# Kernel tuning notes

Measured on AMD Instinct MI355X. Metric: run time of the kernel, lower is better.

Reference implementation:

```python
import jax, jax.numpy as jnp
import numpy as np

B, N, C = 4, 2048, 512
H, D, L = 8, 64, 64  # num_heads, per-head dim, lunchbox_dim
SCALE = max(D, L) ** (-0.5)

def setup_inputs() -> dict:
    key = jax.random.key(0)
    k1, k2, k3, k4 = jax.random.split(key, 4)
    x = jax.random.normal(k1, (B, N, C), dtype=jnp.float32)
    v = jax.random.normal(k2, (N, H, L), dtype=jnp.float32) * (1.0 / np.sqrt(N))
    qkv = jax.random.normal(k3, (C, D * 2 * H), dtype=jnp.float32) * (1.0 / np.sqrt(C))
    proj = jax.random.normal(k4, (H * L, D), dtype=jnp.float32) * (1.0 / np.sqrt(H * L))
    return {"x": x, "v": v, "qkv": qkv, "proj": proj}

def reference(x, v, qkv, proj):
    # x: [B,N,C] -> [B,N,H,2,D]
    h = jnp.einsum('bnc,cd->bnd', x, qkv).reshape(B, N, H, 2, D)
    q = h[:, :, :, 0, :]  # [B,N,H,D]
    k = h[:, :, :, 1, :]  # [B,N,H,D]
    # attention scores [B,H,N,N]; NOTE: original code calls tf.nn.softmax but
    # discards the result, so no softmax is applied (faithful reproduction).
    attn = jnp.einsum('bnhd,bmhd->bhnm', q, k) * SCALE
    # contract with batch-independent lunchbox V: [B,H,N,N] x [N,H,L] -> [B,N,H,L]
    res = jnp.einsum('bhnm,mhl->bnhl', attn, v).reshape(B, N, H * L)
    out = jnp.einsum('bnc,cd->bnd', res, proj)  # [B,N,D]
    return out
```

## Files before the change

### kernel.cpp

```cpp
#include <hip/hip_runtime.h>
#include <hip/hip_bf16.h>


using f32x4 = __attribute__((ext_vector_type(4))) float;
using s16x8 = __attribute__((ext_vector_type(8))) short;

__device__ __forceinline__ unsigned short f2bf(float f) {
  unsigned int i;
  __builtin_memcpy(&i, &f, 4);
  unsigned int lsb = (i >> 16) & 1u;
  i += 0x7fffu + lsb;
  return (unsigned short)(i >> 16);
}
__device__ __forceinline__ float bf2f(unsigned short u) {
  unsigned int i = ((unsigned int)u) << 16;
  float f;
  __builtin_memcpy(&f, &i, 4);
  return f;
}
__device__ __forceinline__ void async_cp16(const void* g, void* l) {
  __builtin_amdgcn_global_load_lds((const __attribute__((address_space(1))) void*)g,
                                   (__attribute__((address_space(3))) void*)l, 16, 0, 0);
}

__global__ void k_convert_x(const float* __restrict__ x, unsigned short* __restrict__ xb) {
  size_t i = ((size_t)blockIdx.x * 256 + threadIdx.x) * 8;
  f32x4 a = *(const f32x4*)(x + i);
  f32x4 b = *(const f32x4*)(x + i + 4);
  ushort4 lo, hi;
  lo.x = f2bf(a[0]); lo.y = f2bf(a[1]); lo.z = f2bf(a[2]); lo.w = f2bf(a[3]);
  hi.x = f2bf(b[0]); hi.y = f2bf(b[1]); hi.z = f2bf(b[2]); hi.w = f2bf(b[3]);
  *(ushort4*)(xb + i) = lo;
  *(ushort4*)(xb + i + 4) = hi;
}

__global__ void k_transpose_qkv(const float* __restrict__ qkv,
                                unsigned short* __restrict__ qkvT) {
  __shared__ float tile[32][33];
  int j0 = blockIdx.x * 32;
  int c0 = blockIdx.y * 32;
  int tx = threadIdx.x, ty = threadIdx.y;
#pragma unroll
  for (int i = 0; i < 32; i += 8)
    tile[ty + i][tx] = qkv[(size_t)(c0 + ty + i) * 1024 + j0 + tx];
  __syncthreads();
  int h = j0 >> 7, s = (j0 >> 6) & 1, d0 = j0 & 63;
  int jp0 = s * 512 + h * 64 + d0;
#pragma unroll
  for (int i = 0; i < 32; i += 8)
    qkvT[(size_t)(jp0 + ty + i) * 512 + c0 + tx] = f2bf(tile[tx][ty + i]);
}

__global__ void k_gemm1(const unsigned short* __restrict__ A,
                        const unsigned short* __restrict__ Bt,
                        unsigned short* __restrict__ Qws,
                        unsigned short* __restrict__ Kws) {
  __shared__ unsigned short As[128 * 64];
  __shared__ unsigned short Bs[128 * 64];
  const int m0 = blockIdx.x * 128;
  const int n0 = blockIdx.y * 128;
  const int tid = threadIdx.x;
  const int lane = tid & 63;
  const int wave = tid >> 6;
  const int wm = wave >> 1, wn = wave & 1;

  f32x4 acc[4][4] = {};

  const int rstage = wave * 32 + (lane >> 3);
  const int cstage = (lane & 7) * 8;

  for (int kt = 0; kt < 512; kt += 64) {
    __syncthreads();
#pragma unroll
    for (int i = 0; i < 4; ++i) {
      async_cp16(A + (size_t)(m0 + rstage + i * 8) * 512 + kt + cstage,
                 As + (wave * 32 + i * 8) * 64);
      async_cp16(Bt + (size_t)(n0 + rstage + i * 8) * 512 + kt + cstage,
                 Bs + (wave * 32 + i * 8) * 64);
    }
    __syncthreads();
#pragma unroll
    for (int kk = 0; kk < 64; kk += 32) {
      s16x8 af[4], bfr[4];
#pragma unroll
      for (int i = 0; i < 4; ++i)
        af[i] = *(const s16x8*)(As + (wm * 64 + i * 16 + (lane & 15)) * 64 + kk + (lane >> 4) * 8);
#pragma unroll
      for (int j = 0; j < 4; ++j)
        bfr[j] = *(const s16x8*)(Bs + (wn * 64 + j * 16 + (lane & 15)) * 64 + kk + (lane >> 4) * 8);
#pragma unroll
      for (int i = 0; i < 4; ++i)
#pragma unroll
        for (int j = 0; j < 4; ++j)
          acc[i][j] = __builtin_amdgcn_mfma_f32_16x16x32_bf16(af[i], bfr[j], acc[i][j], 0, 0, 0);
    }
  }
  const int n_base = n0 + wn * 64;
#pragma unroll
  for (int i = 0; i < 4; ++i) {
    int grow = m0 + wm * 64 + i * 16 + (lane >> 4) * 4;
#pragma unroll
    for (int j = 0; j < 4; ++j) {
      int gcol = n_base + j * 16 + (lane & 15);
      unsigned short* dst;
      float scale;
      if (gcol < 512) { dst = Qws; scale = 0.125f; }
      else            { dst = Kws; gcol -= 512; scale = 1.0f; }
#pragma unroll
      for (int r = 0; r < 4; ++r)
        dst[(size_t)(grow + r) * 512 + gcol] = f2bf(acc[i][j][r] * scale);
    }
  }
}

__global__ void k_kv_partial(const unsigned short* __restrict__ Kws,
                             const float* __restrict__ v,
                             float* __restrict__ KVp) {
  const int wg = blockIdx.x;
  const int chunk = wg & 15;
  const int h = (wg >> 4) & 7;
  const int b = wg >> 7;
  __shared__ unsigned short Ks[128 * 64];
  __shared__ float Vs[128 * 64];
  const int tid = threadIdx.x;
  const int lane = tid & 63;
  const int wave = tid >> 6;
  const int n0 = chunk * 128;
  {
    const int r = wave * 32 + (lane >> 3);
    const int c = (lane & 7) * 8;
#pragma unroll
    for (int i = 0; i < 4; ++i)
      async_cp16(Kws + (size_t)(b * 2048 + n0 + r + i * 8) * 512 + h * 64 + c,
                 Ks + (wave * 32 + i * 8) * 64);
  }
  {
    const int r = wave * 32 + (lane >> 4);
    const int c = (lane & 15) * 4;
#pragma unroll
    for (int i = 0; i < 8; ++i)
      async_cp16(v + (size_t)(n0 + r + i * 4) * 512 + h * 64 + c,
                 Vs + (wave * 32 + i * 4) * 64);
  }
  __syncthreads();
  const int dq0 = (tid & 15) * 4;
  const int l0 = (tid >> 4) * 4;
  float acc[4][4] = {};
#pragma unroll 4
  for (int n = 0; n < 128; ++n) {
    ushort4 ku = *(const ushort4*)(Ks + n * 64 + dq0);
    f32x4 va = *(const f32x4*)(Vs + n * 64 + l0);
    float ka[4] = {bf2f(ku.x), bf2f(ku.y), bf2f(ku.z), bf2f(ku.w)};
#pragma unroll
    for (int a = 0; a < 4; ++a)
#pragma unroll
      for (int c = 0; c < 4; ++c)
        acc[a][c] += ka[a] * va[c];
  }
  float* dst = KVp + (size_t)wg * 4096;
#pragma unroll
  for (int a = 0; a < 4; ++a) {
    f32x4 o;
    o[0] = acc[a][0]; o[1] = acc[a][1]; o[2] = acc[a][2]; o[3] = acc[a][3];
    *(f32x4*)(dst + (dq0 + a) * 64 + l0) = o;
  }
}

__global__ void k_kv_reduce_w(const float* __restrict__ KVp,
                              const float* __restrict__ proj,
                              unsigned short* __restrict__ WcatT) {
  const int bh = blockIdx.x;
  const int h = bh & 7;
  const int b = bh >> 3;
  __shared__ float kv[64 * 65];
  __shared__ float pj[64 * 64];
  const int tid = threadIdx.x;
#pragma unroll
  for (int j = 0; j < 16; ++j) {
    int e = tid + j * 256;
    float s = 0.f;
#pragma unroll
    for (int c = 0; c < 16; ++c)
      s += KVp[((size_t)bh * 16 + c) * 4096 + e];
    kv[(e >> 6) * 65 + (e & 63)] = s;
  }
#pragma unroll
  for (int j = 0; j < 16; ++j) {
    int e = tid + j * 256;
    pj[e] = proj[(size_t)(h * 64 + (e >> 6)) * 64 + (e & 63)];
  }
  __syncthreads();
  const int dq = tid >> 2;
  const int d0 = (tid & 3) * 16;
  f32x4 w[4] = {};
  for (int l = 0; l < 64; ++l) {
    float kvv = kv[dq * 65 + l];
#pragma unroll
    for (int jj = 0; jj < 4; ++jj) {
      f32x4 p4 = *(const f32x4*)(pj + l * 64 + d0 + jj * 4);
      w[jj] += kvv * p4;
    }
  }
#pragma unroll
  for (int jj = 0; jj < 4; ++jj)
#pragma unroll
    for (int q = 0; q < 4; ++q)
      WcatT[(size_t)(b * 64 + d0 + jj * 4 + q) * 512 + h * 64 + dq] = f2bf(w[jj][q]);
}

__global__ void k_gemm2(const unsigned short* __restrict__ Qws,
                        const unsigned short* __restrict__ WcatT,
                        float* __restrict__ out) {
  const int mt = blockIdx.x;
  const int b = blockIdx.y;
  const int m0 = b * 2048 + mt * 128;
  __shared__ unsigned short As[128 * 64];
  __shared__ unsigned short Bs[64 * 64];
  const int tid = threadIdx.x;
  const int lane = tid & 63;
  const int wave = tid >> 6;
  const int rstage = wave * 32 + (lane >> 3);
  const int cstage = (lane & 7) * 8;
  f32x4 acc[2][4] = {};
  const unsigned short* Bb = WcatT + (size_t)b * 64 * 512;
  for (int kt = 0; kt < 512; kt += 64) {
    __syncthreads();
#pragma unroll
    for (int i = 0; i < 4; ++i)
      async_cp16(Qws + (size_t)(m0 + rstage + i * 8) * 512 + kt + cstage,
                 As + (wave * 32 + i * 8) * 64);
#pragma unroll
    for (int i = 0; i < 2; ++i)
      async_cp16(Bb + (size_t)(wave * 16 + i * 8 + (lane >> 3)) * 512 + kt + cstage,
                 Bs + (wave * 16 + i * 8) * 64);
    __syncthreads();
#pragma unroll
    for (int kk = 0; kk < 64; kk += 32) {
      s16x8 af[2], bfr[4];
#pragma unroll
      for (int i = 0; i < 2; ++i)
        af[i] = *(const s16x8*)(As + (wave * 32 + i * 16 + (lane & 15)) * 64 + kk + (lane >> 4) * 8);
#pragma unroll
      for (int j = 0; j < 4; ++j)
        bfr[j] = *(const s16x8*)(Bs + (j * 16 + (lane & 15)) * 64 + kk + (lane >> 4) * 8);
#pragma unroll
      for (int i = 0; i < 2; ++i)
#pragma unroll
        for (int j = 0; j < 4; ++j)
          acc[i][j] = __builtin_amdgcn_mfma_f32_16x16x32_bf16(af[i], bfr[j], acc[i][j], 0, 0, 0);
    }
  }
#pragma unroll
  for (int i = 0; i < 2; ++i) {
    int grow = m0 + wave * 32 + i * 16 + (lane >> 4) * 4;
#pragma unroll
    for (int j = 0; j < 4; ++j) {
      int gcol = j * 16 + (lane & 15);
#pragma unroll
      for (int r = 0; r < 4; ++r)
        out[(size_t)(grow + r) * 64 + gcol] = acc[i][j][r];
    }
  }
}

extern "C" void kernel_launch(void* const* d_in, const int* in_sizes, int n_in,
                              void* d_out, int out_size, void* d_ws, size_t ws_size,
                              hipStream_t stream) {
  const float* x    = (const float*)d_in[0];
  const float* v    = (const float*)d_in[1];
  const float* qkv  = (const float*)d_in[2];
  const float* proj = (const float*)d_in[3];
  float* out = (float*)d_out;

  char* ws = (char*)d_ws;
  unsigned short* xb   = (unsigned short*)ws; ws += (size_t)8192 * 512 * 2;
  unsigned short* qkvT = (unsigned short*)ws; ws += (size_t)1024 * 512 * 2;
  unsigned short* Qws  = (unsigned short*)ws; ws += (size_t)8192 * 512 * 2;
  unsigned short* Kws  = (unsigned short*)ws; ws += (size_t)8192 * 512 * 2;
  float*          KVp  = (float*)ws;          ws += (size_t)512 * 4096 * 4;
  unsigned short* Wc   = (unsigned short*)ws; ws += (size_t)4 * 64 * 512 * 2;

  hipLaunchKernelGGL(k_convert_x, dim3(2048), dim3(256), 0, stream, x, xb);
  hipLaunchKernelGGL(k_transpose_qkv, dim3(32, 16), dim3(32, 8), 0, stream, qkv, qkvT);
  hipLaunchKernelGGL(k_gemm1, dim3(64, 8), dim3(256), 0, stream, xb, qkvT, Qws, Kws);
  hipLaunchKernelGGL(k_kv_partial, dim3(512), dim3(256), 0, stream, Kws, v, KVp);
  hipLaunchKernelGGL(k_kv_reduce_w, dim3(32), dim3(256), 0, stream, KVp, proj, Wc);
  hipLaunchKernelGGL(k_gemm2, dim3(16, 4), dim3(256), 0, stream, Qws, Wc, out);
}
```

Measured before the change: 122.1 us.

## Merge prep kernels, double gemm1 waves, and split gemm2 into single-wave tiles

Fuses the x conversion and qkv transpose into one launch, removing a kernel launch gap. gemm1 now runs 8 waves per block, each owning a 32x64 sub-tile instead of 64x64, which halves accumulator registers and is meant to raise occupancy. gemm2 is rewritten as 512 single-wave blocks that read operands straight from global memory with no LDS staging, trading shared-memory reuse for many more parallel blocks to fill the GPU.

```diff
diff --git a/kernel.cpp b/kernel.cpp
--- a/kernel.cpp
+++ b/kernel.cpp
@@ -23,38 +23,42 @@
                                    (__attribute__((address_space(3))) void*)l, 16, 0, 0);
 }
 
-__global__ void k_convert_x(const float* __restrict__ x, unsigned short* __restrict__ xb) {
-  size_t i = ((size_t)blockIdx.x * 256 + threadIdx.x) * 8;
-  f32x4 a = *(const f32x4*)(x + i);
-  f32x4 b = *(const f32x4*)(x + i + 4);
-  ushort4 lo, hi;
-  lo.x = f2bf(a[0]); lo.y = f2bf(a[1]); lo.z = f2bf(a[2]); lo.w = f2bf(a[3]);
-  hi.x = f2bf(b[0]); hi.y = f2bf(b[1]); hi.z = f2bf(b[2]); hi.w = f2bf(b[3]);
-  *(ushort4*)(xb + i) = lo;
-  *(ushort4*)(xb + i + 4) = hi;
-}
-
-__global__ void k_transpose_qkv(const float* __restrict__ qkv,
-                                unsigned short* __restrict__ qkvT) {
-  __shared__ float tile[32][33];
-  int j0 = blockIdx.x * 32;
-  int c0 = blockIdx.y * 32;
-  int tx = threadIdx.x, ty = threadIdx.y;
-#pragma unroll
-  for (int i = 0; i < 32; i += 8)
-    tile[ty + i][tx] = qkv[(size_t)(c0 + ty + i) * 1024 + j0 + tx];
-  __syncthreads();
-  int h = j0 >> 7, s = (j0 >> 6) & 1, d0 = j0 & 63;
-  int jp0 = s * 512 + h * 64 + d0;
-#pragma unroll
-  for (int i = 0; i < 32; i += 8)
-    qkvT[(size_t)(jp0 + ty + i) * 512 + c0 + tx] = f2bf(tile[tx][ty + i]);
-}
-
-__global__ void k_gemm1(const unsigned short* __restrict__ A,
-                        const unsigned short* __restrict__ Bt,
-                        unsigned short* __restrict__ Qws,
-                        unsigned short* __restrict__ Kws) {
+__global__ void k_prep(const float* __restrict__ x, const float* __restrict__ qkv,
+                       unsigned short* __restrict__ xb, unsigned short* __restrict__ qkvT) {
+  const int id = blockIdx.x;
+  const int tid = threadIdx.x;
+  if (id < 2048) {
+    size_t i = ((size_t)id * 256 + tid) * 8;
+    f32x4 a = *(const f32x4*)(x + i);
+    f32x4 b = *(const f32x4*)(x + i + 4);
+    ushort4 lo, hi;
+    lo.x = f2bf(a[0]); lo.y = f2bf(a[1]); lo.z = f2bf(a[2]); lo.w = f2bf(a[3]);
+    hi.x = f2bf(b[0]); hi.y = f2bf(b[1]); hi.z = f2bf(b[2]); hi.w = f2bf(b[3]);
+    *(ushort4*)(xb + i) = lo;
+    *(ushort4*)(xb + i + 4) = hi;
+  } else {
+    __shared__ float tile[32][33];
+    const int idx = id - 2048;
+    const int j0 = (idx & 31) * 32;
+    const int c0 = (idx >> 5) * 32;
+    const int tx = tid & 31, ty = tid >> 5;
+#pragma unroll
+    for (int i = 0; i < 32; i += 8)
+      tile[ty + i][tx] = qkv[(size_t)(c0 + ty + i) * 1024 + j0 + tx];
+    __syncthreads();
+    const int h = j0 >> 7, s = (j0 >> 6) & 1, d0 = j0 & 63;
+    const int jp0 = s * 512 + h * 64 + d0;
+#pragma unroll
+    for (int i = 0; i < 32; i += 8)
+      qkvT[(size_t)(jp0 + ty + i) * 512 + c0 + tx] = f2bf(tile[tx][ty + i]);
+  }
+}
+
+__global__ __launch_bounds__(512) void k_gemm1(
+    const unsigned short* __restrict__ A,
+    const unsigned short* __restrict__ Bt,
+    unsigned short* __restrict__ Qws,
+    unsigned short* __restrict__ Kws) {
   __shared__ unsigned short As[128 * 64];
   __shared__ unsigned short Bs[128 * 64];
   const int m0 = blockIdx.x * 128;
@@ -64,32 +68,32 @@
   const int wave = tid >> 6;
   const int wm = wave >> 1, wn = wave & 1;
 
-  f32x4 acc[4][4] = {};
-
-  const int rstage = wave * 32 + (lane >> 3);
-  const int cstage = (lane & 7) * 8;
+  f32x4 acc[2][4] = {};
+
+  const int rlane = lane >> 3;
+  const int clane = (lane & 7) * 8;
 
   for (int kt = 0; kt < 512; kt += 64) {
     __syncthreads();
 #pragma unroll
-    for (int i = 0; i < 4; ++i) {
-      async_cp16(A + (size_t)(m0 + rstage + i * 8) * 512 + kt + cstage,
-                 As + (wave * 32 + i * 8) * 64);
-      async_cp16(Bt + (size_t)(n0 + rstage + i * 8) * 512 + kt + cstage,
-                 Bs + (wave * 32 + i * 8) * 64);
+    for (int i = 0; i < 2; ++i) {
+      async_cp16(A + (size_t)(m0 + i * 64 + wave * 8 + rlane) * 512 + kt + clane,
+                 As + (i * 64 + wave * 8) * 64);
+      async_cp16(Bt + (size_t)(n0 + i * 64 + wave * 8 + rlane) * 512 + kt + clane,
+                 Bs + (i * 64 + wave * 8) * 64);
     }
     __syncthreads();
 #pragma unroll
     for (int kk = 0; kk < 64; kk += 32) {
-      s16x8 af[4], bfr[4];
-#pragma unroll
-      for (int i = 0; i < 4; ++i)
-        af[i] = *(const s16x8*)(As + (wm * 64 + i * 16 + (lane & 15)) * 64 + kk + (lane >> 4) * 8);
+      s16x8 af[2], bfr[4];
+#pragma unroll
+      for (int i = 0; i < 2; ++i)
+        af[i] = *(const s16x8*)(As + (wm * 32 + i * 16 + (lane & 15)) * 64 + kk + (lane >> 4) * 8);
 #pragma unroll
       for (int j = 0; j < 4; ++j)
         bfr[j] = *(const s16x8*)(Bs + (wn * 64 + j * 16 + (lane & 15)) * 64 + kk + (lane >> 4) * 8);
 #pragma unroll
-      for (int i = 0; i < 4; ++i)
+      for (int i = 0; i < 2; ++i)
 #pragma unroll
         for (int j = 0; j < 4; ++j)
           acc[i][j] = __builtin_amdgcn_mfma_f32_16x16x32_bf16(af[i], bfr[j], acc[i][j], 0, 0, 0);
@@ -97,8 +101,8 @@
   }
   const int n_base = n0 + wn * 64;
 #pragma unroll
-  for (int i = 0; i < 4; ++i) {
-    int grow = m0 + wm * 64 + i * 16 + (lane >> 4) * 4;
+  for (int i = 0; i < 2; ++i) {
+    int grow = m0 + wm * 32 + i * 16 + (lane >> 4) * 4;
 #pragma unroll
     for (int j = 0; j < 4; ++j) {
       int gcol = n_base + j * 16 + (lane & 15);
@@ -208,58 +212,32 @@
       WcatT[(size_t)(b * 64 + d0 + jj * 4 + q) * 512 + h * 64 + dq] = f2bf(w[jj][q]);
 }
 
-__global__ void k_gemm2(const unsigned short* __restrict__ Qws,
-                        const unsigned short* __restrict__ WcatT,
-                        float* __restrict__ out) {
-  const int mt = blockIdx.x;
-  const int b = blockIdx.y;
-  const int m0 = b * 2048 + mt * 128;
-  __shared__ unsigned short As[128 * 64];
-  __shared__ unsigned short Bs[64 * 64];
-  const int tid = threadIdx.x;
-  const int lane = tid & 63;
-  const int wave = tid >> 6;
-  const int rstage = wave * 32 + (lane >> 3);
-  const int cstage = (lane & 7) * 8;
-  f32x4 acc[2][4] = {};
-  const unsigned short* Bb = WcatT + (size_t)b * 64 * 512;
-  for (int kt = 0; kt < 512; kt += 64) {
-    __syncthreads();
-#pragma unroll
-    for (int i = 0; i < 4; ++i)
-      async_cp16(Qws + (size_t)(m0 + rstage + i * 8) * 512 + kt + cstage,
-                 As + (wave * 32 + i * 8) * 64);
-#pragma unroll
-    for (int i = 0; i < 2; ++i)
-      async_cp16(Bb + (size_t)(wave * 16 + i * 8 + (lane >> 3)) * 512 + kt + cstage,
-                 Bs + (wave * 16 + i * 8) * 64);
-    __syncthreads();
-#pragma unroll
-    for (int kk = 0; kk < 64; kk += 32) {
-      s16x8 af[2], bfr[4];
-#pragma unroll
-      for (int i = 0; i < 2; ++i)
-        af[i] = *(const s16x8*)(As + (wave * 32 + i * 16 + (lane & 15)) * 64 + kk + (lane >> 4) * 8);
-#pragma unroll
-      for (int j = 0; j < 4; ++j)
-        bfr[j] = *(const s16x8*)(Bs + (j * 16 + (lane & 15)) * 64 + kk + (lane >> 4) * 8);
-#pragma unroll
-      for (int i = 0; i < 2; ++i)
-#pragma unroll
-        for (int j = 0; j < 4; ++j)
-          acc[i][j] = __builtin_amdgcn_mfma_f32_16x16x32_bf16(af[i], bfr[j], acc[i][j], 0, 0, 0);
-    }
-  }
-#pragma unroll
-  for (int i = 0; i < 2; ++i) {
-    int grow = m0 + wave * 32 + i * 16 + (lane >> 4) * 4;
+__global__ __launch_bounds__(64) void k_gemm2(
+    const unsigned short* __restrict__ Qws,
+    const unsigned short* __restrict__ WcatT,
+    float* __restrict__ out) {
+  const int m0 = blockIdx.x * 16;
+  const int lane = threadIdx.x;
+  const unsigned short* Bb = WcatT + (size_t)(m0 >> 11) * 64 * 512;
+  const int arow = lane & 15;
+  const int koff = (lane >> 4) * 8;
+  f32x4 acc[4] = {};
+#pragma unroll
+  for (int kk = 0; kk < 16; ++kk) {
+    s16x8 af = *(const s16x8*)(Qws + (size_t)(m0 + arow) * 512 + kk * 32 + koff);
 #pragma unroll
     for (int j = 0; j < 4; ++j) {
-      int gcol = j * 16 + (lane & 15);
-#pragma unroll
-      for (int r = 0; r < 4; ++r)
-        out[(size_t)(grow + r) * 64 + gcol] = acc[i][j][r];
-    }
+      s16x8 bf = *(const s16x8*)(Bb + (size_t)(j * 16 + arow) * 512 + kk * 32 + koff);
+      acc[j] = __builtin_amdgcn_mfma_f32_16x16x32_bf16(af, bf, acc[j], 0, 0, 0);
+    }
+  }
+  const int grow = m0 + (lane >> 4) * 4;
+#pragma unroll
+  for (int j = 0; j < 4; ++j) {
+    int gcol = j * 16 + arow;
+#pragma unroll
+    for (int r = 0; r < 4; ++r)
+      out[(size_t)(grow + r) * 64 + gcol] = acc[j][r];
   }
 }
 
@@ -280,10 +258,9 @@
   float*          KVp  = (float*)ws;          ws += (size_t)512 * 4096 * 4;
   unsigned short* Wc   = (unsigned short*)ws; ws += (size_t)4 * 64 * 512 * 2;
 
-  hipLaunchKernelGGL(k_convert_x, dim3(2048), dim3(256), 0, stream, x, xb);
-  hipLaunchKernelGGL(k_transpose_qkv, dim3(32, 16), dim3(32, 8), 0, stream, qkv, qkvT);
-  hipLaunchKernelGGL(k_gemm1, dim3(64, 8), dim3(256), 0, stream, xb, qkvT, Qws, Kws);
+  hipLaunchKernelGGL(k_prep, dim3(2560), dim3(256), 0, stream, x, qkv, xb, qkvT);
+  hipLaunchKernelGGL(k_gemm1, dim3(64, 8), dim3(512), 0, stream, xb, qkvT, Qws, Kws);
   hipLaunchKernelGGL(k_kv_partial, dim3(512), dim3(256), 0, stream, Kws, v, KVp);
   hipLaunchKernelGGL(k_kv_reduce_w, dim3(32), dim3(256), 0, stream, KVp, proj, Wc);
-  hipLaunchKernelGGL(k_gemm2, dim3(16, 4), dim3(256), 0, stream, Qws, Wc, out);
-}
+  hipLaunchKernelGGL(k_gemm2, dim3(512), dim3(64), 0, stream, Qws, Wc, out);
+}
```

After: 118.7 us. 1.03x faster.
